# Performance work log

Measured on AMD Instinct MI355X. Metric: run time of the kernel, lower is better.

Reference implementation:

```python
import jax, jax.numpy as jnp
import numpy as np
from jax.scipy.special import logsumexp

SINKHORN_ITERS = 3
EPS = 1e-12


def setup_inputs() -> dict:
    key = jax.random.key(0)
    ks = jax.random.split(key, 10)
    B, C, H, W = 32, 384, 48, 48
    HID, D, K = 512, 128, 64
    s = 0.05
    return {
        "x": jax.random.normal(ks[0], (B, C, H, W), dtype=jnp.float32),
        # cluster_features branch: 1x1 convs == per-pixel matmuls
        "w1": jax.random.normal(ks[1], (HID, C), dtype=jnp.float32) * s,
        "b1": jax.random.normal(ks[2], (HID,), dtype=jnp.float32) * s,
        "w2": jax.random.normal(ks[3], (D, HID), dtype=jnp.float32) * s,
        "b2": jax.random.normal(ks[4], (D,), dtype=jnp.float32) * s,
        # score branch
        "s1": jax.random.normal(ks[5], (HID, C), dtype=jnp.float32) * s,
        "c1": jax.random.normal(ks[6], (HID,), dtype=jnp.float32) * s,
        "s2": jax.random.normal(ks[7], (K, HID), dtype=jnp.float32) * s,
        "c2": jax.random.normal(ks[8], (K,), dtype=jnp.float32) * s,
        "alpha": jnp.asarray(1.0, dtype=jnp.float32),  # dust_bin
    }


def _log_optimal_transport(scores, alpha, iters):
    # scores: [b, m, n] with m = num_clusters, n = num tokens
    b, m, n = scores.shape
    norm = -jnp.log(jnp.asarray(m + n, dtype=scores.dtype))
    bins = jnp.broadcast_to(alpha, (b, 1, n)).astype(scores.dtype)
    Z = jnp.concatenate([scores, bins], axis=1)  # [b, m+1, n]
    log_mu = jnp.concatenate([
        jnp.full((m,), norm, dtype=scores.dtype),
        jnp.log(jnp.asarray(n - m, dtype=scores.dtype))[None] + norm,
    ])  # [m+1]
    log_nu = jnp.full((n,), norm, dtype=scores.dtype)
    log_mu = jnp.broadcast_to(log_mu, (b, m + 1))
    log_nu = jnp.broadcast_to(log_nu, (b, n))

    u = jnp.zeros_like(log_mu)
    v = jnp.zeros_like(log_nu)
    for _ in range(iters):
        u = log_mu - logsumexp(Z + v[:, None, :], axis=2)
        v = log_nu - logsumexp(Z + u[:, :, None], axis=1)
    return Z + u[:, :, None] + v[:, None, :] - norm


def reference(x, w1, b1, w2, b2, s1, c1, s2, c2, alpha):
    B, C, H, W = x.shape
    xf = x.reshape(B, C, H * W)  # [b, c, n]
    # cluster features: 1x1 conv -> relu -> 1x1 conv (dropout is identity in eval)
    h = jnp.maximum(jnp.einsum('oc,bcn->bon', w1, xf) + b1[:, None], 0.0)
    f = jnp.einsum('oc,bcn->bon', w2, h) + b2[:, None]  # [b, D, n]
    # scores
    hs = jnp.maximum(jnp.einsum('oc,bcn->bon', s1, xf) + c1[:, None], 0.0)
    p = jnp.einsum('oc,bcn->bon', s2, hs) + c2[:, None]  # [b, K, n]
    # log-domain optimal transport with dust bin
    Z = _log_optimal_transport(p, alpha, SINKHORN_ITERS)
    P = jnp.exp(Z)[:, :-1, :]  # [b, K, n], drop dust bin row
    # repeat-mul-sum pooling == batched contraction over tokens
    agg = jnp.einsum('bdn,bkn->bdk', f, P)  # [b, D, K]
    nrm = jnp.sqrt(jnp.sum(agg * agg, axis=1, keepdims=True))
    agg = agg / jnp.maximum(nrm, EPS)  # L2 normalize over cluster_dim
    return agg.reshape(B, -1)  # [b, D*K]
```

## Files before the change

### kernel.cpp

```cpp
#include <hip/hip_runtime.h>
#include <math.h>
#include <stdint.h>

#define HW_N 2304
#define CB   384
#define HIDD 512
#define HID2 1024
#define DD   128
#define KK   64
#define BATCH 32
#define M1   65
#define NTOK (BATCH * HW_N)
#define NORM_ARG 2368.0f

typedef __bf16 bf16;
typedef __bf16 bf16x8 __attribute__((ext_vector_type(8)));
typedef float  f32x4  __attribute__((ext_vector_type(4)));

__device__ __forceinline__ void gld16(void* lds, const void* g) {
    __builtin_amdgcn_global_load_lds(
        (const __attribute__((address_space(1))) uint32_t*)g,
        (__attribute__((address_space(3))) uint32_t*)lds, 16, 0, 0);
}

template<int N> __device__ __forceinline__ void waitvm() {
    if constexpr (N == 0) asm volatile("s_waitcnt vmcnt(0)" ::: "memory");
    else if constexpr (N == 3) asm volatile("s_waitcnt vmcnt(3)" ::: "memory");
    else if constexpr (N == 4) asm volatile("s_waitcnt vmcnt(4)" ::: "memory");
    else if constexpr (N == 8) asm volatile("s_waitcnt vmcnt(8)" ::: "memory");
}

__global__ __launch_bounds__(256)
void x_to_bf16T(const float* __restrict__ x, bf16* __restrict__ xT)
{
    const int b  = blockIdx.z;
    const int n0 = blockIdx.x * 64;
    const int c0 = blockIdx.y * 64;
    __shared__ float t[64][65];
    const int tx = threadIdx.x & 15, ty = threadIdx.x >> 4;
    const float* xb = x + (long)b * CB * HW_N;
    #pragma unroll
    for (int r = 0; r < 64; r += 16) {
        const float4 vv = *(const float4*)&xb[(long)(c0 + r + ty) * HW_N + n0 + tx * 4];
        t[r + ty][tx * 4 + 0] = vv.x; t[r + ty][tx * 4 + 1] = vv.y;
        t[r + ty][tx * 4 + 2] = vv.z; t[r + ty][tx * 4 + 3] = vv.w;
    }
    __syncthreads();
    bf16* ob = xT + (long)b * HW_N * CB;
    #pragma unroll
    for (int r = 0; r < 64; r += 16) {
        const int n = r + ty;
        union { bf16 h[4]; uint2 u2; } pk;
        pk.h[0] = (bf16)t[tx * 4 + 0][n]; pk.h[1] = (bf16)t[tx * 4 + 1][n];
        pk.h[2] = (bf16)t[tx * 4 + 2][n]; pk.h[3] = (bf16)t[tx * 4 + 3][n];
        *(uint2*)&ob[(long)(n0 + n) * CB + c0 + tx * 4] = pk.u2;
    }
}

__global__ __launch_bounds__(256)
void f2bf4(const float* __restrict__ in, bf16* __restrict__ out, int n4)
{
    int i = blockIdx.x * 256 + threadIdx.x;
    if (i < n4) {
        float4 vv = ((const float4*)in)[i];
        union { bf16 h[4]; uint2 u2; } pk;
        pk.h[0] = (bf16)vv.x; pk.h[1] = (bf16)vv.y;
        pk.h[2] = (bf16)vv.z; pk.h[3] = (bf16)vv.w;
        ((uint2*)out)[i] = pk.u2;
    }
}

__global__ __launch_bounds__(256)
void concat_bias(const float* __restrict__ b1, const float* __restrict__ c1,
                 float* __restrict__ bc)
{
    int i = blockIdx.x * 256 + threadIdx.x;
    if (i < HIDD) bc[i] = b1[i];
    else if (i < HID2) bc[i] = c1[i - HIDD];
}

template<int FA, int FB, int BK, int OUT_MODE, bool RELU, int MINW>
__global__ __launch_bounds__(512, MINW)
void mfma_gemm8(const bf16* __restrict__ A, int lda,
                const bf16* __restrict__ B, int ldb,
                const float* __restrict__ bias,
                void* __restrict__ OUT, int ldo,
                int K, int nA)
{
    constexpr int BA = 2 * FA * 16;
    constexpr int BB = 4 * FB * 16;
    constexpr int KS = BK / 32;
    constexpr int ROWB = BK * 2;
    constexpr int RPC  = 1024 / ROWB;
    constexpr int LPR  = ROWB / 16;
    constexpr int GA = (BA * ROWB) / 8192;
    constexpr int GB = (BB * ROWB) / 8192;
    constexpr int GAB = GA + GB;

    __shared__ __align__(16) bf16 As[2][BA * BK];
    __shared__ __align__(16) bf16 Bs[2][BB * BK];

    int L = blockIdx.x;
    { const int cpx = gridDim.x >> 3; L = (L & 7) * cpx + (L >> 3); }
    const int ta = L % nA;
    const int tb = L / nA;

    const int tid  = threadIdx.x;
    const int lane = tid & 63;
    const int w    = tid >> 6;
    const int wr   = w >> 2;
    const int wc   = w & 3;

    const char* Ap = (const char*)A + (long)ta * BA * lda * 2;
    const char* Bp = (const char*)B + (long)tb * BB * ldb * 2;
    const long ldab = (long)lda * 2, ldbb = (long)ldb * 2;

    const int subrow = lane / LPR;
    const int cslot  = lane % LPR;
    const int colb   = (BK == 64) ? ((cslot ^ (subrow & 7)) << 4) : (cslot << 4);

    const int rl = lane & 15, q = lane >> 4;
    int koff[KS];
    #pragma unroll
    for (int ks = 0; ks < KS; ++ks)
        koff[ks] = (BK == 64) ? ((((ks << 2) | q) ^ (rl & 7)) << 4) : (q << 4);

    f32x4 acc[FA][FB];
    #pragma unroll
    for (int i = 0; i < FA; i++)
        #pragma unroll
        for (int j = 0; j < FB; j++)
            acc[i][j] = (f32x4){0.f, 0.f, 0.f, 0.f};

    const int nsteps = K / BK;

    auto stageA = [&](int buf, int kt) {
        #pragma unroll
        for (int g = 0; g < GA; ++g) {
            const int row = (g * 8 + w) * RPC + subrow;
            gld16((char*)As[buf] + (g * 8 + w) * 1024,
                  Ap + (long)row * ldab + (long)kt * ROWB + colb);
        }
    };
    auto stageB = [&](int buf, int kt) {
        #pragma unroll
        for (int g = 0; g < GB; ++g) {
            const int row = (g * 8 + w) * RPC + subrow;
            gld16((char*)Bs[buf] + (g * 8 + w) * 1024,
                  Bp + (long)row * ldbb + (long)kt * ROWB + colb);
        }
    };

    stageA(0, 0); stageB(0, 0);
    stageA(1, 1); stageB(1, 1);
    waitvm<GAB>();
    __builtin_amdgcn_s_barrier();

    for (int t = 0; t < nsteps; ++t) {
        const int cur = t & 1;
        const char* Ab = (const char*)As[cur];
        const char* Bb = (const char*)Bs[cur];

        #pragma unroll
        for (int ks = 0; ks < KS; ++ks) {
            bf16x8 a[FA], bb[FB];
            #pragma unroll
            for (int i = 0; i < FA; i++) {
                const int row = wr * FA * 16 + i * 16 + rl;
                a[i] = *(const bf16x8*)(Ab + row * ROWB + koff[ks]);
            }
            #pragma unroll
            for (int j = 0; j < FB; j++) {
                const int row = wc * FB * 16 + j * 16 + rl;
                bb[j] = *(const bf16x8*)(Bb + row * ROWB + koff[ks]);
            }
            __builtin_amdgcn_s_setprio(1);
            #pragma unroll
            for (int i = 0; i < FA; i++)
                #pragma unroll
                for (int j = 0; j < FB; j++)
                    acc[i][j] = __builtin_amdgcn_mfma_f32_16x16x32_bf16(a[i], bb[j], acc[i][j], 0, 0, 0);
            __builtin_amdgcn_s_setprio(0);
        }

        asm volatile("s_waitcnt lgkmcnt(0)" ::: "memory");
        __builtin_amdgcn_s_barrier();
        if (t + 2 < nsteps) { stageA(cur, t + 2); stageB(cur, t + 2); }
        if (t + 1 < nsteps) {
            if (t + 2 < nsteps) waitvm<GAB>(); else waitvm<0>();
            __builtin_amdgcn_s_barrier();
        }
    }

    const int fr = lane & 15;
    const int fq = lane >> 4;

    if (OUT_MODE == 0) {
        #pragma unroll
        for (int i = 0; i < FA; i++) {
            const int ra0 = ta * BA + wr * FA * 16 + i * 16 + fq * 4;
            const float4 bv = *(const float4*)&bias[ra0];
            #pragma unroll
            for (int j = 0; j < FB; j++) {
                const int rb = tb * BB + wc * FB * 16 + j * 16 + fr;
                union { bf16 h[4]; uint2 u2; } pk;
                float v0 = acc[i][j][0] + bv.x, v1 = acc[i][j][1] + bv.y;
                float v2 = acc[i][j][2] + bv.z, v3 = acc[i][j][3] + bv.w;
                if (RELU) {
                    v0 = fmaxf(v0, 0.f); v1 = fmaxf(v1, 0.f);
                    v2 = fmaxf(v2, 0.f); v3 = fmaxf(v3, 0.f);
                }
                pk.h[0] = (bf16)v0; pk.h[1] = (bf16)v1;
                pk.h[2] = (bf16)v2; pk.h[3] = (bf16)v3;
                *(uint2*)&((bf16*)OUT)[(long)rb * ldo + ra0] = pk.u2;
            }
        }
    } else {
        #pragma unroll
        for (int i = 0; i < FA; i++) {
            const int g0 = ta * BA + wr * FA * 16 + i * 16 + fq * 4;
            const int bi = g0 / HW_N;
            const int nn = g0 - bi * HW_N;
            #pragma unroll
            for (int j = 0; j < FB; j++) {
                const int mg = tb * BB + wc * FB * 16 + j * 16 + fr;
                const float bvs = bias[mg];
                float v0 = acc[i][j][0] + bvs, v1 = acc[i][j][1] + bvs;
                float v2 = acc[i][j][2] + bvs, v3 = acc[i][j][3] + bvs;
                if (RELU) {
                    v0 = fmaxf(v0, 0.f); v1 = fmaxf(v1, 0.f);
                    v2 = fmaxf(v2, 0.f); v3 = fmaxf(v3, 0.f);
                }
                const long base = ((long)bi * ldo + mg) * HW_N + nn;
                if (OUT_MODE == 1) {
                    union { bf16 h[4]; uint2 u2; } pk;
                    pk.h[0] = (bf16)v0; pk.h[1] = (bf16)v1;
                    pk.h[2] = (bf16)v2; pk.h[3] = (bf16)v3;
                    *(uint2*)&((bf16*)OUT)[base] = pk.u2;
                } else {
                    *(float4*)&((float*)OUT)[base] = make_float4(v0, v1, v2, v3);
                }
            }
        }
    }
}

template<bool FIRST>
__global__ __launch_bounds__(256)
void sink_u(const float* __restrict__ Z, const float* __restrict__ v,
            const float* __restrict__ alpha, float* __restrict__ u)
{
    const int b = blockIdx.y;
    const int i = blockIdx.x * 4 + (threadIdx.x >> 6);
    if (i > KK) return;
    const int lane = threadIdx.x & 63;
    const float* zr = Z + ((long)b * KK + i) * HW_N;
    const float* vb = v + (long)b * HW_N;
    const float a = alpha[0];
    float m = -INFINITY, s = 0.f;
    for (int j = lane; j < HW_N; j += 64) {
        float val = (i < KK) ? zr[j] : a;
        if (!FIRST) val += vb[j];
        float mn = fmaxf(m, val);
        s = s * __expf(m - mn) + __expf(val - mn);
        m = mn;
    }
    #pragma unroll
    for (int off = 32; off; off >>= 1) {
        float m2 = __shfl_xor(m, off), s2 = __shfl_xor(s, off);
        float mn = fmaxf(m, m2);
        s = s * __expf(m - mn) + s2 * __expf(m2 - mn);
        m = mn;
    }
    if (lane == 0) {
        const float norm = -logf(NORM_ARG);
        const float logmu = (i < KK) ? norm : (logf((float)(HW_N - KK)) + norm);
        u[b * M1 + i] = logmu - (m + __logf(s));
    }
}

__global__ __launch_bounds__(64)
void sink_v(const float* __restrict__ Z, const float* __restrict__ u,
            const float* __restrict__ alpha, float* __restrict__ v)
{
    const int b = blockIdx.y;
    const int n = blockIdx.x * 64 + threadIdx.x;
    const float* ub = u + b * M1;
    const float* Zb = Z + (long)b * KK * HW_N;
    float m = alpha[0] + ub[KK];
    float s = 1.f;
    for (int i = 0; i < KK; i++) {
        float t = Zb[(long)i * HW_N + n] + ub[i];
        float mn = fmaxf(m, t);
        s = s * __expf(m - mn) + __expf(t - mn);
        m = mn;
    }
    const float norm = -logf(NORM_ARG);
    v[(long)b * HW_N + n] = norm - (m + __logf(s));
}

__global__ __launch_bounds__(256)
void agg_partial(const bf16* __restrict__ f, const float* __restrict__ Z,
                 const float* __restrict__ u, const float* __restrict__ v,
                 float* __restrict__ part)
{
    const int c = blockIdx.x;
    const int b = blockIdx.y;
    const int n0 = c << 8;
    const float norm = -logf(NORM_ARG);

    __shared__ float Fs[16][132];
    __shared__ float Ps[16][68];

    const bf16*  fb = f + (long)b * DD * HW_N;
    const float* Zb = Z + (long)b * KK * HW_N;
    const float* ub = u + b * M1;
    const float* vb = v + (long)b * HW_N;

    const int tid = threadIdx.x;
    const int td = tid & 31;
    const int tk = tid >> 5;

    float acc[4][8] = {};

    for (int nt = 0; nt < 256; nt += 16) {
        #pragma unroll
        for (int i = 0; i < 8; i++) {
            int li = tid + (i << 8);
            int d = li >> 4, nn = li & 15;
            Fs[nn][d] = (float)fb[(long)d * HW_N + n0 + nt + nn];
        }
        #pragma unroll
        for (int i = 0; i < 4; i++) {
            int li = tid + (i << 8);
            int k = li >> 4, nn = li & 15;
            int n = n0 + nt + nn;
            Ps[nn][k] = __expf(Zb[(long)k * HW_N + n] + ub[k] + vb[n] - norm);
        }
        __syncthreads();
        #pragma unroll
        for (int nn = 0; nn < 16; nn++) {
            const float4 av = *reinterpret_cast<const float4*>(&Fs[nn][td << 2]);
            const float4 p0 = *reinterpret_cast<const float4*>(&Ps[nn][tk << 3]);
            const float4 p1 = *reinterpret_cast<const float4*>(&Ps[nn][(tk << 3) + 4]);
            float a[4] = {av.x, av.y, av.z, av.w};
            float p[8] = {p0.x, p0.y, p0.z, p0.w, p1.x, p1.y, p1.z, p1.w};
            #pragma unroll
            for (int i = 0; i < 4; i++)
                #pragma unroll
                for (int j = 0; j < 8; j++)
                    acc[i][j] += a[i] * p[j];
        }
        __syncthreads();
    }

    float* pb = part + (long)(b * 9 + c) * (DD * KK);
    #pragma unroll
    for (int i = 0; i < 4; i++) {
        int d = (td << 2) + i;
        float4 o0 = make_float4(acc[i][0], acc[i][1], acc[i][2], acc[i][3]);
        float4 o1 = make_float4(acc[i][4], acc[i][5], acc[i][6], acc[i][7]);
        *reinterpret_cast<float4*>(&pb[d * KK + (tk << 3)]) = o0;
        *reinterpret_cast<float4*>(&pb[d * KK + (tk << 3) + 4]) = o1;
    }
}

__global__ __launch_bounds__(256)
void finalize(const float* __restrict__ part, float* __restrict__ out)
{
    const int b = blockIdx.x;
    __shared__ float agg[DD * KK];
    __shared__ float nrm[KK];
    const int tid = threadIdx.x;

    for (int idx = tid; idx < DD * KK; idx += 256) {
        float s = 0.f;
        #pragma unroll
        for (int cc = 0; cc < 9; cc++)
            s += part[(long)(b * 9 + cc) * (DD * KK) + idx];
        agg[idx] = s;
    }
    __syncthreads();
    if (tid < KK) {
        float ss = 0.f;
        for (int d = 0; d < DD; d++) { float t = agg[d * KK + tid]; ss += t * t; }
        nrm[tid] = fmaxf(sqrtf(ss), 1e-12f);
    }
    __syncthreads();
    for (int idx = tid; idx < DD * KK; idx += 256)
        out[(long)b * (DD * KK) + idx] = agg[idx] / nrm[idx & 63];
}

extern "C" void kernel_launch(void* const* d_in, const int* in_sizes, int n_in,
                              void* d_out, int out_size, void* d_ws, size_t ws_size,
                              hipStream_t stream)
{
    const float* x     = (const float*)d_in[0];
    const float* w1    = (const float*)d_in[1];
    const float* b1    = (const float*)d_in[2];
    const float* w2    = (const float*)d_in[3];
    const float* b2    = (const float*)d_in[4];
    const float* s1    = (const float*)d_in[5];
    const float* c1    = (const float*)d_in[6];
    const float* s2    = (const float*)d_in[7];
    const float* c2    = (const float*)d_in[8];
    const float* alpha = (const float*)d_in[9];
    float* out = (float*)d_out;

    char* p = (char*)d_ws;
    bf16* Wc  = (bf16*)p;  p += (long)HID2 * CB * 2;
    bf16* w2b = (bf16*)p;  p += (long)DD * HIDD * 2;
    bf16* s2b = (bf16*)p;  p += (long)KK * HIDD * 2;
    float* bc = (float*)p; p += (long)HID2 * 4;
    bf16* xT  = (bf16*)p;  p += (long)NTOK * CB * 2;
    bf16* hs  = (bf16*)p;  p += (long)NTOK * HID2 * 2;
    bf16* f   = (bf16*)p;  p += (long)BATCH * DD * HW_N * 2;
    float* Z  = (float*)p; p += (long)BATCH * KK * HW_N * 4;
    float* u  = (float*)p; p += (long)BATCH * M1 * 4;
    float* v  = (float*)p; p += (long)BATCH * HW_N * 4;
    float* part = (float*)p;

    f2bf4<<<(HIDD * CB / 4 + 255) / 256, 256, 0, stream>>>(w1, Wc, HIDD * CB / 4);
    f2bf4<<<(HIDD * CB / 4 + 255) / 256, 256, 0, stream>>>(s1, Wc + (long)HIDD * CB, HIDD * CB / 4);
    f2bf4<<<(DD * HIDD / 4 + 255) / 256, 256, 0, stream>>>(w2, w2b, DD * HIDD / 4);
    f2bf4<<<(KK * HIDD / 4 + 255) / 256, 256, 0, stream>>>(s2, s2b, KK * HIDD / 4);
    concat_bias<<<4, 256, 0, stream>>>(b1, c1, bc);

    x_to_bf16T<<<dim3(36, 6, 32), 256, 0, stream>>>(x, xT);

    mfma_gemm8<8, 4, 32, 0, true, 2><<<1152, 512, 0, stream>>>(
        Wc, CB, xT, CB, bc, hs, HID2, CB, HID2 / 256);

    mfma_gemm8<4, 2, 64, 1, false, 4><<<NTOK / 128, 512, 0, stream>>>(
        hs, HID2, w2b, HIDD, b2, f, DD, HIDD, NTOK / 128);

    mfma_gemm8<4, 1, 64, 2, false, 4><<<NTOK / 128, 512, 0, stream>>>(
        hs + HIDD, HID2, s2b, HIDD, c2, Z, KK, HIDD, NTOK / 128);

    sink_u<true ><<<dim3(17, 32), 256, 0, stream>>>(Z, v, alpha, u);
    sink_v<<<dim3(36, 32), 64, 0, stream>>>(Z, u, alpha, v);
    sink_u<false><<<dim3(17, 32), 256, 0, stream>>>(Z, v, alpha, u);
    sink_v<<<dim3(36, 32), 64, 0, stream>>>(Z, u, alpha, v);
    sink_u<false><<<dim3(17, 32), 256, 0, stream>>>(Z, v, alpha, u);
    sink_v<<<dim3(36, 32), 64, 0, stream>>>(Z, u, alpha, v);

    agg_partial<<<dim3(9, 32), 256, 0, stream>>>(f, Z, u, v, part);
    finalize<<<32, 256, 0, stream>>>(part, out);
}
```

Baseline: 326.7 us.

## Replace 512-thread GEMM with 256-thread smaller-tile GEMM and fuse weight prep

Replaces the 8-wave templated GEMM, which has a configurable K-step and XOR-swizzled LDS, with a 4-wave variant that uses a fixed 32-wide K-step and smaller 128x128 / 128x64 tiles. The first GEMM now launches 4608 blocks instead of 1152. The five weight and bias conversion launches are merged into one prep kernel, and w2/s2 are packed into one buffer. The goal is higher occupancy and lower launch overhead. The trade-off is less data reuse per tile, more K-loop barriers, and possible LDS bank conflicts because the swizzle is gone.

```diff
diff --git a/kernel.cpp b/kernel.cpp
--- a/kernel.cpp
+++ b/kernel.cpp
@@ -25,9 +25,13 @@
 
 template<int N> __device__ __forceinline__ void waitvm() {
     if constexpr (N == 0) asm volatile("s_waitcnt vmcnt(0)" ::: "memory");
+    else if constexpr (N == 1) asm volatile("s_waitcnt vmcnt(1)" ::: "memory");
+    else if constexpr (N == 2) asm volatile("s_waitcnt vmcnt(2)" ::: "memory");
     else if constexpr (N == 3) asm volatile("s_waitcnt vmcnt(3)" ::: "memory");
     else if constexpr (N == 4) asm volatile("s_waitcnt vmcnt(4)" ::: "memory");
-    else if constexpr (N == 8) asm volatile("s_waitcnt vmcnt(8)" ::: "memory");
+    else if constexpr (N == 5) asm volatile("s_waitcnt vmcnt(5)" ::: "memory");
+    else if constexpr (N == 6) asm volatile("s_waitcnt vmcnt(6)" ::: "memory");
+    else asm volatile("s_waitcnt vmcnt(8)" ::: "memory");
 }
 
 __global__ __launch_bounds__(256)
@@ -57,48 +61,58 @@
     }
 }
 
+__device__ __forceinline__ void cvtq(const float* __restrict__ in,
+                                     bf16* __restrict__ out, int q)
+{
+    float4 vv = ((const float4*)in)[q];
+    union { bf16 h[4]; uint2 u2; } pk;
+    pk.h[0] = (bf16)vv.x; pk.h[1] = (bf16)vv.y;
+    pk.h[2] = (bf16)vv.z; pk.h[3] = (bf16)vv.w;
+    ((uint2*)out)[q] = pk.u2;
+}
+
 __global__ __launch_bounds__(256)
-void f2bf4(const float* __restrict__ in, bf16* __restrict__ out, int n4)
-{
+void prep_weights(const float* __restrict__ w1, const float* __restrict__ s1,
+                  const float* __restrict__ w2, const float* __restrict__ s2,
+                  const float* __restrict__ b1, const float* __restrict__ c1,
+                  bf16* __restrict__ Wc, bf16* __restrict__ Wf,
+                  float* __restrict__ bc)
+{
+    const int QW1 = HIDD * CB / 4;
+    const int QW2 = DD * HIDD / 4;
+    const int QS2 = KK * HIDD / 4;
     int i = blockIdx.x * 256 + threadIdx.x;
-    if (i < n4) {
-        float4 vv = ((const float4*)in)[i];
-        union { bf16 h[4]; uint2 u2; } pk;
-        pk.h[0] = (bf16)vv.x; pk.h[1] = (bf16)vv.y;
-        pk.h[2] = (bf16)vv.z; pk.h[3] = (bf16)vv.w;
-        ((uint2*)out)[i] = pk.u2;
-    }
-}
-
-__global__ __launch_bounds__(256)
-void concat_bias(const float* __restrict__ b1, const float* __restrict__ c1,
-                 float* __restrict__ bc)
-{
-    int i = blockIdx.x * 256 + threadIdx.x;
-    if (i < HIDD) bc[i] = b1[i];
-    else if (i < HID2) bc[i] = c1[i - HIDD];
-}
-
-template<int FA, int FB, int BK, int OUT_MODE, bool RELU, int MINW>
-__global__ __launch_bounds__(512, MINW)
-void mfma_gemm8(const bf16* __restrict__ A, int lda,
+    if (i < QW1)                       { cvtq(w1, Wc, i); return; }
+    i -= QW1;
+    if (i < QW1)                       { cvtq(s1, Wc + (long)HIDD * CB, i); return; }
+    i -= QW1;
+    if (i < QW2)                       { cvtq(w2, Wf, i); return; }
+    i -= QW2;
+    if (i < QS2)                       { cvtq(s2, Wf + (long)DD * HIDD, i); return; }
+    i -= QS2;
+    if (i < 256) {
+        float4 vv = (i < 128) ? ((const float4*)b1)[i] : ((const float4*)c1)[i - 128];
+        ((float4*)bc)[i] = vv;
+    }
+}
+
+template<int FA, int FB, int OUT_MODE, bool RELU, int MINW>
+__global__ __launch_bounds__(256, MINW)
+void mfma_gemm4(const bf16* __restrict__ A, int lda,
                 const bf16* __restrict__ B, int ldb,
                 const float* __restrict__ bias,
                 void* __restrict__ OUT, int ldo,
                 int K, int nA)
 {
     constexpr int BA = 2 * FA * 16;
-    constexpr int BB = 4 * FB * 16;
-    constexpr int KS = BK / 32;
-    constexpr int ROWB = BK * 2;
-    constexpr int RPC  = 1024 / ROWB;
-    constexpr int LPR  = ROWB / 16;
-    constexpr int GA = (BA * ROWB) / 8192;
-    constexpr int GB = (BB * ROWB) / 8192;
+    constexpr int BB = 2 * FB * 16;
+    constexpr int ROWB = 64;
+    constexpr int GA = (BA * ROWB) / 4096;
+    constexpr int GB = (BB * ROWB) / 4096;
     constexpr int GAB = GA + GB;
 
-    __shared__ __align__(16) bf16 As[2][BA * BK];
-    __shared__ __align__(16) bf16 Bs[2][BB * BK];
+    __shared__ __align__(16) bf16 As[2][BA * 32];
+    __shared__ __align__(16) bf16 Bs[2][BB * 32];
 
     int L = blockIdx.x;
     { const int cpx = gridDim.x >> 3; L = (L & 7) * cpx + (L >> 3); }
@@ -108,22 +122,16 @@
     const int tid  = threadIdx.x;
     const int lane = tid & 63;
     const int w    = tid >> 6;
-    const int wr   = w >> 2;
-    const int wc   = w & 3;
+    const int wr   = w >> 1, wc = w & 1;
 
     const char* Ap = (const char*)A + (long)ta * BA * lda * 2;
     const char* Bp = (const char*)B + (long)tb * BB * ldb * 2;
     const long ldab = (long)lda * 2, ldbb = (long)ldb * 2;
 
-    const int subrow = lane / LPR;
-    const int cslot  = lane % LPR;
-    const int colb   = (BK == 64) ? ((cslot ^ (subrow & 7)) << 4) : (cslot << 4);
+    const int subrow = lane >> 2;
+    const int colb   = (lane & 3) << 4;
 
     const int rl = lane & 15, q = lane >> 4;
-    int koff[KS];
-    #pragma unroll
-    for (int ks = 0; ks < KS; ++ks)
-        koff[ks] = (BK == 64) ? ((((ks << 2) | q) ^ (rl & 7)) << 4) : (q << 4);
 
     f32x4 acc[FA][FB];
     #pragma unroll
@@ -132,22 +140,22 @@
         for (int j = 0; j < FB; j++)
             acc[i][j] = (f32x4){0.f, 0.f, 0.f, 0.f};
 
-    const int nsteps = K / BK;
+    const int nsteps = K / 32;
 
     auto stageA = [&](int buf, int kt) {
         #pragma unroll
         for (int g = 0; g < GA; ++g) {
-            const int row = (g * 8 + w) * RPC + subrow;
-            gld16((char*)As[buf] + (g * 8 + w) * 1024,
-                  Ap + (long)row * ldab + (long)kt * ROWB + colb);
+            const int ii = g * 4 + w;
+            gld16((char*)As[buf] + ii * 1024,
+                  Ap + (long)(ii * 16 + subrow) * ldab + (long)kt * ROWB + colb);
         }
     };
     auto stageB = [&](int buf, int kt) {
         #pragma unroll
         for (int g = 0; g < GB; ++g) {
-            const int row = (g * 8 + w) * RPC + subrow;
-            gld16((char*)Bs[buf] + (g * 8 + w) * 1024,
-                  Bp + (long)row * ldbb + (long)kt * ROWB + colb);
+            const int ii = g * 4 + w;
+            gld16((char*)Bs[buf] + ii * 1024,
+                  Bp + (long)(ii * 16 + subrow) * ldbb + (long)kt * ROWB + colb);
         }
     };
 
@@ -161,27 +169,21 @@
         const char* Ab = (const char*)As[cur];
         const char* Bb = (const char*)Bs[cur];
 
-        #pragma unroll
-        for (int ks = 0; ks < KS; ++ks) {
-            bf16x8 a[FA], bb[FB];
+        bf16x8 a[FA], bb[FB];
+        #pragma unroll
+        for (int i = 0; i < FA; i++)
+            a[i] = *(const bf16x8*)(Ab + (wr * FA * 16 + i * 16 + rl) * ROWB + (q << 4));
+        #pragma unroll
+        for (int j = 0; j < FB; j++)
+            bb[j] = *(const bf16x8*)(Bb + (wc * FB * 16 + j * 16 + rl) * ROWB + (q << 4));
+
+        __builtin_amdgcn_s_setprio(1);
+        #pragma unroll
+        for (int i = 0; i < FA; i++)
             #pragma unroll
-            for (int i = 0; i < FA; i++) {
-                const int row = wr * FA * 16 + i * 16 + rl;
-                a[i] = *(const bf16x8*)(Ab + row * ROWB + koff[ks]);
-            }
-            #pragma unroll
-            for (int j = 0; j < FB; j++) {
-                const int row = wc * FB * 16 + j * 16 + rl;
-                bb[j] = *(const bf16x8*)(Bb + row * ROWB + koff[ks]);
-            }
-            __builtin_amdgcn_s_setprio(1);
-            #pragma unroll
-            for (int i = 0; i < FA; i++)
-                #pragma unroll
-                for (int j = 0; j < FB; j++)
-                    acc[i][j] = __builtin_amdgcn_mfma_f32_16x16x32_bf16(a[i], bb[j], acc[i][j], 0, 0, 0);
-            __builtin_amdgcn_s_setprio(0);
-        }
+            for (int j = 0; j < FB; j++)
+                acc[i][j] = __builtin_amdgcn_mfma_f32_16x16x32_bf16(a[i], bb[j], acc[i][j], 0, 0, 0);
+        __builtin_amdgcn_s_setprio(0);
 
         asm volatile("s_waitcnt lgkmcnt(0)" ::: "memory");
         __builtin_amdgcn_s_barrier();
@@ -409,8 +411,7 @@
 
     char* p = (char*)d_ws;
     bf16* Wc  = (bf16*)p;  p += (long)HID2 * CB * 2;
-    bf16* w2b = (bf16*)p;  p += (long)DD * HIDD * 2;
-    bf16* s2b = (bf16*)p;  p += (long)KK * HIDD * 2;
+    bf16* Wf  = (bf16*)p;  p += (long)(DD + KK) * HIDD * 2;
     float* bc = (float*)p; p += (long)HID2 * 4;
     bf16* xT  = (bf16*)p;  p += (long)NTOK * CB * 2;
     bf16* hs  = (bf16*)p;  p += (long)NTOK * HID2 * 2;
@@ -420,22 +421,18 @@
     float* v  = (float*)p; p += (long)BATCH * HW_N * 4;
     float* part = (float*)p;
 
-    f2bf4<<<(HIDD * CB / 4 + 255) / 256, 256, 0, stream>>>(w1, Wc, HIDD * CB / 4);
-    f2bf4<<<(HIDD * CB / 4 + 255) / 256, 256, 0, stream>>>(s1, Wc + (long)HIDD * CB, HIDD * CB / 4);
-    f2bf4<<<(DD * HIDD / 4 + 255) / 256, 256, 0, stream>>>(w2, w2b, DD * HIDD / 4);
-    f2bf4<<<(KK * HIDD / 4 + 255) / 256, 256, 0, stream>>>(s2, s2b, KK * HIDD / 4);
-    concat_bias<<<4, 256, 0, stream>>>(b1, c1, bc);
+    prep_weights<<<481, 256, 0, stream>>>(w1, s1, w2, s2, b1, c1, Wc, Wf, bc);
 
     x_to_bf16T<<<dim3(36, 6, 32), 256, 0, stream>>>(x, xT);
 
-    mfma_gemm8<8, 4, 32, 0, true, 2><<<1152, 512, 0, stream>>>(
-        Wc, CB, xT, CB, bc, hs, HID2, CB, HID2 / 256);
-
-    mfma_gemm8<4, 2, 64, 1, false, 4><<<NTOK / 128, 512, 0, stream>>>(
-        hs, HID2, w2b, HIDD, b2, f, DD, HIDD, NTOK / 128);
-
-    mfma_gemm8<4, 1, 64, 2, false, 4><<<NTOK / 128, 512, 0, stream>>>(
-        hs + HIDD, HID2, s2b, HIDD, c2, Z, KK, HIDD, NTOK / 128);
+    mfma_gemm4<4, 4, 0, true, 4><<<4608, 256, 0, stream>>>(
+        Wc, CB, xT, CB, bc, hs, HID2, CB, HID2 / 128);
+
+    mfma_gemm4<4, 4, 1, false, 4><<<NTOK / 128, 256, 0, stream>>>(
+        hs, HID2, Wf, HIDD, b2, f, DD, HIDD, NTOK / 128);
+
+    mfma_gemm4<4, 2, 2, false, 4><<<NTOK / 128, 256, 0, stream>>>(
+        hs + HIDD, HID2, Wf + (long)DD * HIDD, HIDD, c2, Z, KK, HIDD, NTOK / 128);
 
     sink_u<true ><<<dim3(17, 32), 256, 0, stream>>>(Z, v, alpha, u);
     sink_v<<<dim3(36, 32), 64, 0, stream>>>(Z, u, alpha, v);
```

New measurement: 293.2 us. 10.2% less time.
